# Performance work log

Measured on AMD Instinct MI355X. Metric: run time of the kernel, lower is better.

Reference implementation:

```python
import jax, jax.numpy as jnp
import numpy as np

D_IN, H1, H2, H3 = 1024, 512, 256, 128  # embedding MLP dims
D_CBP = 2048                             # compact bilinear pooling output dim
H_C = 1024                               # comparator hidden dim
CLASSES = 10
B = 16384
SLOPE = 0.2  # LeakyReLU negative slope


def _lrelu(x):
    return jnp.where(x >= 0, x, SLOPE * x)


def _embed(x, W1, b1, W2, b2, W3, b3):
    x = _lrelu(x @ W1 + b1)
    x = _lrelu(x @ W2 + b2)
    x = _lrelu(x @ W3 + b3)
    return x  # [B, 128]


def setup_inputs() -> dict:
    key = jax.random.key(0)
    ks = jax.random.split(key, 16)

    def lin(k, fan_in, fan_out):
        bound = 1.0 / np.sqrt(fan_in)
        kw, kb = jax.random.split(k)
        W = jax.random.uniform(kw, (fan_in, fan_out), jnp.float32, -bound, bound)
        b = jax.random.uniform(kb, (fan_out,), jnp.float32, -bound, bound)
        return W, b

    W1, b1 = lin(ks[0], D_IN, H1)
    W2, b2 = lin(ks[1], H1, H2)
    W3, b3 = lin(ks[2], H2, H3)
    Wc1, bc1 = lin(ks[3], D_CBP, H_C)
    Wc2, bc2 = lin(ks[4], H_C, CLASSES)

    X = jax.random.normal(ks[5], (B, D_IN), jnp.float32)
    Centers = jax.random.normal(ks[6], (B, D_IN), jnp.float32)

    # count-sketch hashes (int constants) and +-1 signs (float buffers)
    h1 = jax.random.randint(ks[7], (H3,), 0, D_CBP, jnp.int32)
    h2 = jax.random.randint(ks[8], (H3,), 0, D_CBP, jnp.int32)
    s1 = jnp.sign(jax.random.normal(ks[9], (H3,), jnp.float32)) + (jax.random.normal(ks[9], (H3,)) == 0)
    s2 = jnp.sign(jax.random.normal(ks[10], (H3,), jnp.float32)) + (jax.random.normal(ks[10], (H3,)) == 0)

    return {"X": X, "Centers": Centers,
            "W1": W1, "b1": b1, "W2": W2, "b2": b2, "W3": W3, "b3": b3,
            "h1": h1, "s1": s1, "h2": h2, "s2": s2,
            "Wc1": Wc1, "bc1": bc1, "Wc2": Wc2, "bc2": bc2}


def _cbp(x, y, h1, s1, h2, s2):
    # count-sketch via tiny dense sketch matrices [128, 2048]
    M1 = jnp.zeros((H3, D_CBP), x.dtype).at[jnp.arange(H3), h1].set(s1)
    M2 = jnp.zeros((H3, D_CBP), y.dtype).at[jnp.arange(H3), h2].set(s2)
    sk1 = x @ M1  # [B, 2048]
    sk2 = y @ M2
    # circular convolution via real FFT
    return jnp.fft.irfft(jnp.fft.rfft(sk1, axis=-1) * jnp.fft.rfft(sk2, axis=-1), n=D_CBP, axis=-1)


def reference(X, Centers, W1, b1, W2, b2, W3, b3, h1, s1, h2, s2, Wc1, bc1, Wc2, bc2):
    ex = _embed(X, W1, b1, W2, b2, W3, b3)        # [B, 128]
    ec = _embed(Centers, W1, b1, W2, b2, W3, b3)  # [B, 128]
    cbp = _cbp(ex, ec, h1, s1, h2, s2)            # [B, 2048]
    z = _lrelu(cbp @ Wc1 + bc1)                   # [B, 1024]
    logits = z @ Wc2 + bc2                        # [B, classes]
    return jax.nn.softmax(logits, axis=1)
```

## Files before the change

kernel.cpp:

```cpp
#include <hip/hip_runtime.h>
#include <hip/hip_bf16.h>
#include <math.h>

#define BATCH   16384
#define D_IN    1024
#define H1_DIM  512
#define H2_DIM  256
#define H3_DIM  128
#define D_CBP   2048
#define H_C     1024
#define CLASSES 10
#define SLOPE   0.2f

#define NK_PAD  1088
#define NF      (2 * NK_PAD)
#define NF_USED 2080

typedef short v8s __attribute__((ext_vector_type(8)));
typedef float v4f __attribute__((ext_vector_type(4)));
typedef unsigned short u16;
typedef unsigned int   u32;

__device__ __forceinline__ float b2f(unsigned short u) {
  return __uint_as_float(((unsigned)u) << 16);
}
__device__ __forceinline__ u16 f2b(float f) {
  __hip_bfloat16 h = __float2bfloat16(f);
  return __builtin_bit_cast(unsigned short, h);
}

__device__ __forceinline__ float2 twiddle(int idx) {
  const float ang = 6.2831853071795864769f * (float)idx / 2048.f;
  return make_float2(__cosf(ang), __sinf(ang));
}

__device__ __forceinline__ void g2l16(const void* g, void* l) {
  __builtin_amdgcn_global_load_lds(
      (const __attribute__((address_space(1))) void*)g,
      (__attribute__((address_space(3))) void*)l, 16, 0, 0);
}

__global__ __launch_bounds__(256) void gemm_bf16(
    const u16* __restrict__ A,
    const u16* __restrict__ Bt,
    const float* __restrict__ bias,
    u16* __restrict__ C,
    int M, int N, int K, int lda, int ldb, float slope)
{
  __shared__ __align__(16) short Asb[5][128 * 32];
  __shared__ __align__(16) short Bsb[5][128 * 32];

  const int tid  = threadIdx.x;
  const int wave = tid >> 6, lane = tid & 63;
  const int wm = wave >> 1, wn = wave & 1;
  const int u = lane & 15, quad = lane >> 4;

  const int nwg = gridDim.x * gridDim.y;
  int id = blockIdx.y * gridDim.x + blockIdx.x;
  if ((nwg & 7) == 0) id = (id & 7) * (nwg >> 3) + (id >> 3);
  const int m0 = (id / gridDim.x) * 128, n0 = (id % gridDim.x) * 128;

  const int g_log = ((lane & 3) - ((lane >> 3) & 3)) & 3;
  const int srow  = wave * 32 + (lane >> 2);
  const u16* gA0 = A  + (size_t)(m0 + srow)      * lda + g_log * 8;
  const u16* gA1 = A  + (size_t)(m0 + srow + 16) * lda + g_log * 8;
  const u16* gB0 = Bt + (size_t)(n0 + srow)      * ldb + g_log * 8;
  const u16* gB1 = Bt + (size_t)(n0 + srow + 16) * ldb + g_log * 8;
  const int lo0 = (wave * 32)      * 32;
  const int lo1 = (wave * 32 + 16) * 32;

  const int gran = (quad + (u >> 1)) & 3;
  int offA[4], offB[4];
#pragma unroll
  for (int i = 0; i < 4; ++i) {
    offA[i] = (wm * 64 + i * 16 + u) * 32 + gran * 8;
    offB[i] = (wn * 64 + i * 16 + u) * 32 + gran * 8;
  }

  v4f acc[4][4];
#pragma unroll
  for (int i = 0; i < 4; ++i)
#pragma unroll
    for (int j = 0; j < 4; ++j) acc[i][j] = (v4f){0.f, 0.f, 0.f, 0.f};

  const int nsteps = K >> 5;

  auto stage = [&](int s, int buf) {
    const int k0 = s * 32;
    g2l16(gA0 + k0, &Asb[buf][lo0]);
    g2l16(gA1 + k0, &Asb[buf][lo1]);
    g2l16(gB0 + k0, &Bsb[buf][lo0]);
    g2l16(gB1 + k0, &Bsb[buf][lo1]);
  };

  stage(0, 0);
  if (nsteps > 1) stage(1, 1);
  if (nsteps > 2) stage(2, 2);

  int cb = 0, sb = 3;
  for (int t = 0; t < nsteps; ++t) {
    if (t + 3 < nsteps) stage(t + 3, sb);

    const int rem = nsteps - 1 - t;
    if (rem >= 3)      asm volatile("s_waitcnt vmcnt(12)" ::: "memory");
    else if (rem == 2) asm volatile("s_waitcnt vmcnt(8)"  ::: "memory");
    else if (rem == 1) asm volatile("s_waitcnt vmcnt(4)"  ::: "memory");
    else               asm volatile("s_waitcnt vmcnt(0)"  ::: "memory");
    __builtin_amdgcn_s_barrier();
    asm volatile("" ::: "memory");

    v8s a[4], b[4];
#pragma unroll
    for (int i = 0; i < 4; ++i) a[i] = *(const v8s*)&Asb[cb][offA[i]];
#pragma unroll
    for (int j = 0; j < 4; ++j) b[j] = *(const v8s*)&Bsb[cb][offB[j]];
    __builtin_amdgcn_s_setprio(1);
#pragma unroll
    for (int i = 0; i < 4; ++i)
#pragma unroll
      for (int j = 0; j < 4; ++j)
        acc[i][j] = __builtin_amdgcn_mfma_f32_16x16x32_bf16(a[i], b[j], acc[i][j], 0, 0, 0);
    __builtin_amdgcn_s_setprio(0);

    cb = (cb == 4) ? 0 : cb + 1;
    sb = (sb == 4) ? 0 : sb + 1;
  }

  float bcol[4];
#pragma unroll
  for (int j = 0; j < 4; ++j) bcol[j] = bias[n0 + wn * 64 + j * 16 + u];
#pragma unroll
  for (int i = 0; i < 4; ++i)
#pragma unroll
    for (int r = 0; r < 4; ++r) {
      const size_t ro = (size_t)(m0 + wm * 64 + i * 16 + quad * 4 + r) * N
                        + n0 + wn * 64 + u;
#pragma unroll
      for (int j = 0; j < 4; ++j) {
        float v = acc[i][j][r] + bcol[j];
        v = v >= 0.f ? v : slope * v;
        C[ro + j * 16] = f2b(v);
      }
    }
}

__device__ __forceinline__ void f_pass(
    const u16* gA0, const u16* gA1, const u16* gB0, const u16* gB1,
    short (*Asb)[128 * 32], short (*Bsb)[128 * 32],
    int lo0, int lo1, const int* offA, const int* offB,
    v4f (&acc)[4][4])
{
  auto stage = [&](int s, int buf) {
    const int k0 = s * 32;
    g2l16(gA0 + k0, &Asb[buf][lo0]);
    g2l16(gA1 + k0, &Asb[buf][lo1]);
    g2l16(gB0 + k0, &Bsb[buf][lo0]);
    g2l16(gB1 + k0, &Bsb[buf][lo1]);
  };
  stage(0, 0); stage(1, 1); stage(2, 2);
#pragma unroll
  for (int t = 0; t < 4; ++t) {
    if (t == 0) stage(3, 3);
    if (t == 0)      asm volatile("s_waitcnt vmcnt(12)" ::: "memory");
    else if (t == 1) asm volatile("s_waitcnt vmcnt(8)"  ::: "memory");
    else if (t == 2) asm volatile("s_waitcnt vmcnt(4)"  ::: "memory");
    else             asm volatile("s_waitcnt vmcnt(0)"  ::: "memory");
    __builtin_amdgcn_s_barrier();
    asm volatile("" ::: "memory");
    v8s a[4], b[4];
#pragma unroll
    for (int i = 0; i < 4; ++i) a[i] = *(const v8s*)&Asb[t][offA[i]];
#pragma unroll
    for (int j = 0; j < 4; ++j) b[j] = *(const v8s*)&Bsb[t][offB[j]];
    __builtin_amdgcn_s_setprio(1);
#pragma unroll
    for (int i = 0; i < 4; ++i)
#pragma unroll
      for (int j = 0; j < 4; ++j)
        acc[i][j] = __builtin_amdgcn_mfma_f32_16x16x32_bf16(a[i], b[j], acc[i][j], 0, 0, 0);
    __builtin_amdgcn_s_setprio(0);
  }
}

__global__ __launch_bounds__(256) void gemm_f1f2(
    const u16* __restrict__ E3,
    const u16* __restrict__ C1t,
    const u16* __restrict__ C2t,
    u16* __restrict__ F1)
{
  __shared__ __align__(16) short Asb[5][128 * 32];
  __shared__ __align__(16) short Bsb[5][128 * 32];

  const int tid  = threadIdx.x;
  const int wave = tid >> 6, lane = tid & 63;
  const int wm = wave >> 1, wn = wave & 1;
  const int u = lane & 15, quad = lane >> 4;
  const int N = NF, K = H3_DIM;

  const int nwg = gridDim.x * gridDim.y;
  int id = blockIdx.y * gridDim.x + blockIdx.x;
  if ((nwg & 7) == 0) id = (id & 7) * (nwg >> 3) + (id >> 3);
  const int m0 = (id / gridDim.x) * 128, n0 = (id % gridDim.x) * 128;

  const int g_log = ((lane & 3) - ((lane >> 3) & 3)) & 3;
  const int srow  = wave * 32 + (lane >> 2);
  const size_t aoffX = (size_t)(m0 + srow) * K + g_log * 8;
  const size_t boff  = (size_t)(n0 + srow) * K + g_log * 8;
  const int lo0 = (wave * 32)      * 32;
  const int lo1 = (wave * 32 + 16) * 32;

  const int gran = (quad + (u >> 1)) & 3;
  int offA[4], offB[4];
#pragma unroll
  for (int i = 0; i < 4; ++i) {
    offA[i] = (wm * 64 + i * 16 + u) * 32 + gran * 8;
    offB[i] = (wn * 64 + i * 16 + u) * 32 + gran * 8;
  }

  v4f acc1[4][4], acc2[4][4];
#pragma unroll
  for (int i = 0; i < 4; ++i)
#pragma unroll
    for (int j = 0; j < 4; ++j) {
      acc1[i][j] = (v4f){0.f, 0.f, 0.f, 0.f};
      acc2[i][j] = (v4f){0.f, 0.f, 0.f, 0.f};
    }

  f_pass(E3 + aoffX, E3 + aoffX + (size_t)16 * K,
         C1t + boff, C1t + boff + (size_t)16 * K,
         Asb, Bsb, lo0, lo1, offA, offB, acc1);
  const size_t aoffC = aoffX + (size_t)BATCH * K;
  f_pass(E3 + aoffC, E3 + aoffC + (size_t)16 * K,
         C2t + boff, C2t + boff + (size_t)16 * K,
         Asb, Bsb, lo0, lo1, offA, offB, acc2);

  const bool im = (u & 1);
#pragma unroll
  for (int i = 0; i < 4; ++i)
#pragma unroll
    for (int r = 0; r < 4; ++r) {
      const size_t ro = (size_t)(m0 + wm * 64 + i * 16 + quad * 4 + r) * N
                        + n0 + wn * 64 + u;
#pragma unroll
      for (int j = 0; j < 4; ++j) {
        const float f1v = acc1[i][j][r];
        const float f1p = __shfl_xor(f1v, 1, 64);
        const float f2v = acc2[i][j][r];
        const float f2p = __shfl_xor(f2v, 1, 64);
        const float outv = im ? (f1p * f2v + f1v * f2p)
                              : (f1v * f2v - f1p * f2p);
        F1[ro + j * 16] = f2b(outv);
      }
    }
}

#define CAST_NB   (BATCH * D_IN / 4 / 256)
#define NB_CAST   (2 * CAST_NB)
#define NB_TW1    ((D_IN / 32) * (H1_DIM / 32))
#define NB_TW2    ((H1_DIM / 32) * (H2_DIM / 32))
#define NB_TW3    ((H2_DIM / 32) * (H3_DIM / 32))
#define NB_TWC1   ((D_CBP / 32) * (H_C / 32))
#define NB_TRANS  (NB_TW1 + NB_TW2 + NB_TW3 + NB_TWC1)
#define NB_GENC   (NF * H3_DIM / 256)
#define NB_GENT   (NF)
#define NB_ZB     9
#define NB_PREP   (NB_CAST + NB_TRANS + NB_GENC + NB_GENT + NB_ZB)

__global__ __launch_bounds__(256) void prep_all(
    const float* __restrict__ X, const float* __restrict__ Centers,
    u16* __restrict__ Xb,
    const float* __restrict__ W1, u16* __restrict__ W1t,
    const float* __restrict__ W2, u16* __restrict__ W2t,
    const float* __restrict__ W3, u16* __restrict__ W3t,
    const float* __restrict__ Wc1, u16* __restrict__ Wc1t,
    const int* __restrict__ h1, const float* __restrict__ s1,
    const int* __restrict__ h2, const float* __restrict__ s2,
    u16* __restrict__ C1t, u16* __restrict__ C2t,
    u16* __restrict__ Tt, float* __restrict__ zbias)
{
  __shared__ float tile[32][33];
  int bx = blockIdx.x;
  const int t = threadIdx.x;

  if (bx < NB_CAST) {
    const float* s = (bx < CAST_NB) ? X : Centers;
    const int i = ((bx < CAST_NB) ? bx : bx - CAST_NB) * 256 + t;
    u16* d = Xb + ((bx < CAST_NB) ? 0 : (size_t)BATCH * D_IN);
    const float4 v = ((const float4*)s)[i];
    __align__(8) u16 o[4] = {f2b(v.x), f2b(v.y), f2b(v.z), f2b(v.w)};
    *(uint2*)(d + (size_t)i * 4) = *(uint2*)o;
    return;
  }
  bx -= NB_CAST;

  if (bx < NB_TRANS) {
    const float* W; u16* Wt; int K, N;
    if (bx < NB_TW1)        { W = W1;  Wt = W1t;  K = D_IN;   N = H1_DIM; }
    else if (bx < NB_TW1 + NB_TW2) {
      bx -= NB_TW1;           W = W2;  Wt = W2t;  K = H1_DIM; N = H2_DIM; }
    else if (bx < NB_TW1 + NB_TW2 + NB_TW3) {
      bx -= NB_TW1 + NB_TW2;  W = W3;  Wt = W3t;  K = H2_DIM; N = H3_DIM; }
    else {
      bx -= NB_TW1 + NB_TW2 + NB_TW3;
                              W = Wc1; Wt = Wc1t; K = D_CBP;  N = H_C;    }
    const int nt = N / 32;
    const int k0 = (bx / nt) * 32, n0 = (bx % nt) * 32;
    const int tx = t & 31, ty = t >> 5;
#pragma unroll
    for (int s = 0; s < 4; ++s) {
      const int k = ty * 4 + s;
      tile[k][tx] = W[(size_t)(k0 + k) * N + n0 + tx];
    }
    __syncthreads();
#pragma unroll
    for (int s = 0; s < 4; ++s) {
      const int n = ty * 4 + s;
      Wt[(size_t)(n0 + n) * K + k0 + tx] = f2b(tile[tx][n]);
    }
    return;
  }
  bx -= NB_TRANS;

  if (bx < NB_GENC) {
    const int id = bx * 256 + t;
    const int m = id >> 7, i = id & 127;
    const int k = m >> 1;
    float v1 = 0.f, v2 = 0.f;
    if (m < 2 * (D_CBP / 2 + 1)) {
      const float2 c1 = twiddle((k * h1[i]) & (D_CBP - 1));
      const float2 c2 = twiddle((k * h2[i]) & (D_CBP - 1));
      v1 = (m & 1) ? -s1[i] * c1.y : s1[i] * c1.x;
      v2 = (m & 1) ? -s2[i] * c2.y : s2[i] * c2.x;
    }
    C1t[id] = f2b(v1);
    C2t[id] = f2b(v2);
    return;
  }
  bx -= NB_GENC;

  if (bx < NB_GENT) {
    const int id = bx * 256 + t;
    const int m = id >> 8, q0 = (id & 255) * 8;
    const int k = m >> 1;
    const float sc = ((k == 0) || (k == D_CBP / 2)) ? (1.f / D_CBP)
                                                    : (2.f / D_CBP);
    __align__(16) u16 o[8];
#pragma unroll
    for (int j = 0; j < 8; ++j) {
      float v = 0.f;
      if (m < 2 * (D_CBP / 2 + 1)) {
        const float2 cs = twiddle((k * (q0 + j)) & (D_CBP - 1));
        v = (m & 1) ? -sc * cs.y : sc * cs.x;
      }
      o[j] = f2b(v);
    }
    *(v8s*)&Tt[(size_t)m * D_CBP + q0] = *(v8s*)o;
    return;
  }
  bx -= NB_GENT;

  {
    const int i = bx * 256 + t;
    if (i < NF) zbias[i] = 0.f;
  }
}

__global__ __launch_bounds__(256) void head_softmax(
    const u16* __restrict__ Z, const float* __restrict__ Wc2,
    const float* __restrict__ bc2, float* __restrict__ out)
{
  const int row  = blockIdx.x * 4 + (threadIdx.x >> 6);
  const int lane = threadIdx.x & 63;

  float acc[CLASSES];
#pragma unroll
  for (int c = 0; c < CLASSES; ++c) acc[c] = 0.f;

  const u16* z = Z + (size_t)row * H_C;
  for (int k = lane; k < H_C; k += 64) {
    const float zv = b2f(z[k]);
    const float* w = Wc2 + (size_t)k * CLASSES;
#pragma unroll
    for (int c = 0; c < CLASSES; ++c) acc[c] += zv * w[c];
  }
#pragma unroll
  for (int c = 0; c < CLASSES; ++c) {
#pragma unroll
    for (int off = 32; off > 0; off >>= 1)
      acc[c] += __shfl_down(acc[c], off);
  }
  if (lane == 0) {
    float l[CLASSES], mx = -1e30f;
#pragma unroll
    for (int c = 0; c < CLASSES; ++c) { l[c] = acc[c] + bc2[c]; mx = fmaxf(mx, l[c]); }
    float s = 0.f;
#pragma unroll
    for (int c = 0; c < CLASSES; ++c) { l[c] = __expf(l[c] - mx); s += l[c]; }
    const float inv = 1.f / s;
#pragma unroll
    for (int c = 0; c < CLASSES; ++c) out[(size_t)row * CLASSES + c] = l[c] * inv;
  }
}

extern "C" void kernel_launch(void* const* d_in, const int* in_sizes, int n_in,
                              void* d_out, int out_size, void* d_ws, size_t ws_size,
                              hipStream_t stream) {
  const float* X       = (const float*)d_in[0];
  const float* Centers = (const float*)d_in[1];
  const float* W1      = (const float*)d_in[2];
  const float* b1      = (const float*)d_in[3];
  const float* W2      = (const float*)d_in[4];
  const float* b2      = (const float*)d_in[5];
  const float* W3      = (const float*)d_in[6];
  const float* b3      = (const float*)d_in[7];
  const int*   h1      = (const int*)d_in[8];
  const float* s1      = (const float*)d_in[9];
  const int*   h2      = (const int*)d_in[10];
  const float* s2      = (const float*)d_in[11];
  const float* Wc1     = (const float*)d_in[12];
  const float* bc1     = (const float*)d_in[13];
  const float* Wc2     = (const float*)d_in[14];
  const float* bc2     = (const float*)d_in[15];
  float* out = (float*)d_out;

  char* ws = (char*)d_ws;
  const size_t MB = 1u << 20;
  const size_t KB = 1u << 10;
  u16*    Xb    = (u16*)(ws);
  u16*    FWt   = (u16*)(ws + 8 * MB + 512 * KB);
  u16*    F1    = (u16*)(ws + 13 * MB);
  u16*    E1b   = (u16*)(ws + 64 * MB);
  u16*    Zb    = (u16*)(ws + 81 * MB);
  u16*    E2b   = (u16*)(ws + 96 * MB);
  u16*    Tt    = (u16*)(ws + 96 * MB);
  u16*    E3b   = (u16*)(ws + 113 * MB);
  u16*    W1t   = (u16*)(ws + 121 * MB);
  u16*    W2t   = (u16*)(ws + 122 * MB);
  u16*    W3t   = (u16*)(ws + 122 * MB + 256 * KB);
  u16*    Wc1t  = (u16*)(ws + 122 * MB + 512 * KB);
  u16*    C1t   = (u16*)(ws + 126 * MB + 512 * KB);
  u16*    C2t   = (u16*)(ws + 127 * MB + 64 * KB);
  float*  zbias = (float*)(ws + 127 * MB + 672 * KB);

  const dim3 blk(256);

  prep_all<<<dim3(NB_PREP), blk, 0, stream>>>(
      X, Centers, Xb, W1, W1t, W2, W2t, W3, W3t, Wc1, Wc1t,
      h1, s1, h2, s2, C1t, C2t, Tt, zbias);

  gemm_bf16<<<dim3(H1_DIM / 128, 2 * BATCH / 128), blk, 0, stream>>>(
      Xb, W1t, b1, E1b, 2 * BATCH, H1_DIM, D_IN, D_IN, D_IN, SLOPE);

  gemm_bf16<<<dim3(NF / 128, H_C / 128), blk, 0, stream>>>(
      Wc1t, Tt, zbias, FWt, H_C, NF, D_CBP, D_CBP, D_CBP, 1.0f);

  gemm_bf16<<<dim3(H2_DIM / 128, 2 * BATCH / 128), blk, 0, stream>>>(
      E1b, W2t, b2, E2b, 2 * BATCH, H2_DIM, H1_DIM, H1_DIM, H1_DIM, SLOPE);
  gemm_bf16<<<dim3(H3_DIM / 128, 2 * BATCH / 128), blk, 0, stream>>>(
      E2b, W3t, b3, E3b, 2 * BATCH, H3_DIM, H2_DIM, H2_DIM, H2_DIM, SLOPE);

  gemm_f1f2<<<dim3(NF / 128, BATCH / 128), blk, 0, stream>>>(
      E3b, C1t, C2t, F1);

  gemm_bf16<<<dim3(H_C / 128, BATCH / 128), blk, 0, stream>>>(
      F1, FWt, bc1, Zb, BATCH, H_C, NF_USED, NF, NF, SLOPE);

  head_softmax<<<dim3(BATCH / 4), blk, 0, stream>>>(Zb, Wc2, bc2, out);
}
```

Before: 453.6 us.

## Add 256x256-tile 512-thread bf16 GEMM for the two largest GEMMs

Adds a new GEMM kernel with 256x256 output tiles, 8 waves per block, each wave computing 128x64, and a 4-buffer LDS ring with two-stage prefetch. It replaces the 128x128 kernel for the first embedding layer and the comparator hidden GEMM. The larger tiles raise arithmetic intensity and cut redundant global loads. In exchange they use more LDS (128 KB per block) and more accumulator registers, lower occupancy, and produce fewer blocks, which can worsen wave quantization. The K=2080 case uses 65 steps, which the ring handles.

```diff
diff --git a/kernel.cpp b/kernel.cpp
--- a/kernel.cpp
+++ b/kernel.cpp
@@ -134,6 +134,106 @@
 #pragma unroll
     for (int r = 0; r < 4; ++r) {
       const size_t ro = (size_t)(m0 + wm * 64 + i * 16 + quad * 4 + r) * N
+                        + n0 + wn * 64 + u;
+#pragma unroll
+      for (int j = 0; j < 4; ++j) {
+        float v = acc[i][j][r] + bcol[j];
+        v = v >= 0.f ? v : slope * v;
+        C[ro + j * 16] = f2b(v);
+      }
+    }
+}
+
+__global__ __launch_bounds__(512) void gemm256_bf16(
+    const u16* __restrict__ A,
+    const u16* __restrict__ Bt,
+    const float* __restrict__ bias,
+    u16* __restrict__ C,
+    int M, int N, int K, int lda, int ldb, float slope)
+{
+  __shared__ __align__(16) short Asb[4][256 * 32];
+  __shared__ __align__(16) short Bsb[4][256 * 32];
+
+  const int tid  = threadIdx.x;
+  const int wave = tid >> 6, lane = tid & 63;
+  const int wm = wave >> 2, wn = wave & 3;
+  const int u = lane & 15, quad = lane >> 4;
+
+  const int nwg = gridDim.x * gridDim.y;
+  int id = blockIdx.y * gridDim.x + blockIdx.x;
+  if ((nwg & 7) == 0) id = (id & 7) * (nwg >> 3) + (id >> 3);
+  const int m0 = (id / gridDim.x) * 256, n0 = (id % gridDim.x) * 256;
+
+  const int g_log = ((lane & 3) - ((lane >> 3) & 3)) & 3;
+  const int srow  = wave * 32 + (lane >> 2);
+  const u16* gA0 = A  + (size_t)(m0 + srow)      * lda + g_log * 8;
+  const u16* gA1 = A  + (size_t)(m0 + srow + 16) * lda + g_log * 8;
+  const u16* gB0 = Bt + (size_t)(n0 + srow)      * ldb + g_log * 8;
+  const u16* gB1 = Bt + (size_t)(n0 + srow + 16) * ldb + g_log * 8;
+  const int lo0 = (wave * 32)      * 32;
+  const int lo1 = (wave * 32 + 16) * 32;
+
+  const int gran = (quad + (u >> 1)) & 3;
+  int offA[8], offB[4];
+#pragma unroll
+  for (int i = 0; i < 8; ++i)
+    offA[i] = (wm * 128 + i * 16 + u) * 32 + gran * 8;
+#pragma unroll
+  for (int j = 0; j < 4; ++j)
+    offB[j] = (wn * 64 + j * 16 + u) * 32 + gran * 8;
+
+  v4f acc[8][4];
+#pragma unroll
+  for (int i = 0; i < 8; ++i)
+#pragma unroll
+    for (int j = 0; j < 4; ++j) acc[i][j] = (v4f){0.f, 0.f, 0.f, 0.f};
+
+  const int nsteps = K >> 5;
+
+  auto stage = [&](int s, int buf) {
+    const int k0 = s * 32;
+    g2l16(gA0 + k0, &Asb[buf][lo0]);
+    g2l16(gA1 + k0, &Asb[buf][lo1]);
+    g2l16(gB0 + k0, &Bsb[buf][lo0]);
+    g2l16(gB1 + k0, &Bsb[buf][lo1]);
+  };
+
+  stage(0, 0);
+  if (nsteps > 1) stage(1, 1);
+
+  for (int t = 0; t < nsteps; ++t) {
+    if (t + 2 < nsteps) stage(t + 2, (t + 2) & 3);
+
+    const int rem = nsteps - 1 - t;
+    if (rem >= 2)      asm volatile("s_waitcnt vmcnt(8)" ::: "memory");
+    else if (rem == 1) asm volatile("s_waitcnt vmcnt(4)" ::: "memory");
+    else               asm volatile("s_waitcnt vmcnt(0)" ::: "memory");
+    __builtin_amdgcn_s_barrier();
+    asm volatile("" ::: "memory");
+
+    const int cb = t & 3;
+    v8s a[8], b[4];
+#pragma unroll
+    for (int i = 0; i < 8; ++i) a[i] = *(const v8s*)&Asb[cb][offA[i]];
+#pragma unroll
+    for (int j = 0; j < 4; ++j) b[j] = *(const v8s*)&Bsb[cb][offB[j]];
+    __builtin_amdgcn_s_setprio(1);
+#pragma unroll
+    for (int i = 0; i < 8; ++i)
+#pragma unroll
+      for (int j = 0; j < 4; ++j)
+        acc[i][j] = __builtin_amdgcn_mfma_f32_16x16x32_bf16(a[i], b[j], acc[i][j], 0, 0, 0);
+    __builtin_amdgcn_s_setprio(0);
+  }
+
+  float bcol[4];
+#pragma unroll
+  for (int j = 0; j < 4; ++j) bcol[j] = bias[n0 + wn * 64 + j * 16 + u];
+#pragma unroll
+  for (int i = 0; i < 8; ++i)
+#pragma unroll
+    for (int r = 0; r < 4; ++r) {
+      const size_t ro = (size_t)(m0 + wm * 128 + i * 16 + quad * 4 + r) * N
                         + n0 + wn * 64 + u;
 #pragma unroll
       for (int j = 0; j < 4; ++j) {
@@ -442,13 +542,13 @@
   u16*    C2t   = (u16*)(ws + 127 * MB + 64 * KB);
   float*  zbias = (float*)(ws + 127 * MB + 672 * KB);
 
-  const dim3 blk(256);
+  const dim3 blk(256), blk512(512);
 
   prep_all<<<dim3(NB_PREP), blk, 0, stream>>>(
       X, Centers, Xb, W1, W1t, W2, W2t, W3, W3t, Wc1, Wc1t,
       h1, s1, h2, s2, C1t, C2t, Tt, zbias);
 
-  gemm_bf16<<<dim3(H1_DIM / 128, 2 * BATCH / 128), blk, 0, stream>>>(
+  gemm256_bf16<<<dim3(H1_DIM / 256, 2 * BATCH / 256), blk512, 0, stream>>>(
       Xb, W1t, b1, E1b, 2 * BATCH, H1_DIM, D_IN, D_IN, D_IN, SLOPE);
 
   gemm_bf16<<<dim3(NF / 128, H_C / 128), blk, 0, stream>>>(
@@ -462,7 +562,7 @@
   gemm_f1f2<<<dim3(NF / 128, BATCH / 128), blk, 0, stream>>>(
       E3b, C1t, C2t, F1);
 
-  gemm_bf16<<<dim3(H_C / 128, BATCH / 128), blk, 0, stream>>>(
+  gemm256_bf16<<<dim3(H_C / 256, BATCH / 256), blk512, 0, stream>>>(
       F1, FWt, bc1, Zb, BATCH, H_C, NF_USED, NF, NF, SLOPE);
 
   head_softmax<<<dim3(BATCH / 4), blk, 0, stream>>>(Zb, Wc2, bc2, out);
```

Measured after the change: 433.4 us. 4.5% less time.
